# Optimization experiments

Measured on AMD Instinct MI355X. Metric: run time of the kernel, lower is better.

## Reference

```python
import jax, jax.numpy as jnp
import numpy as np

B, K = 524288, 64
CUTOFF = jnp.arange(K + 1, dtype=jnp.float32)  # len K+1
S0 = jnp.exp(jnp.float32(-4.0))                # s0 = exp(s0_init)
S = jnp.float32(2.0)                           # logit scale
M = jnp.float32(0.1)                           # margin
SIZE_LOSS = 'average'


def _get_labels(y, e):
    # bin b such that cutoff[b] <= y < cutoff[b+1]
    b = jnp.searchsorted(CUTOFF, y, side='right') - 1          # [B]
    valid = (b >= 0) & (b < K)                                 # [B]
    ar = jnp.arange(K)
    onehot = ar[None, :] == b[:, None]                         # event: single bin
    tail = ar[None, :] >= b[:, None]                           # censored: bin and all later bins
    count = jnp.where(e[:, None] != 0, onehot, tail) & valid[:, None]
    return count.astype(jnp.float32)                           # [B, K] in {0,1}


def setup_inputs() -> dict:
    key = jax.random.key(0)
    k1, k2, k3 = jax.random.split(key, 3)
    inp = jax.random.normal(k1, (B, K), dtype=jnp.float32)
    y = jax.random.uniform(k2, (B,), dtype=jnp.float32, minval=0.0, maxval=float(K))
    e = jax.random.randint(k3, (B,), 0, 2).astype(jnp.int32)
    return {'input': inp, 'y': y, 'e': e}


def reference(input, y, e):
    count = _get_labels(y, e)                                  # [B, K]
    # margin added where count[j] == min(count) (the 'negative' bins)
    min_c = jnp.min(count, axis=1, keepdims=True)
    logits = (input + M * (count == min_c).astype(input.dtype)) * S
    rev = 1.0 - count
    pe = jnp.exp(-logits)                                      # exp(-x)
    pen = jnp.exp(logits)                                      # exp(x)
    correct = jnp.sum(pe * count, axis=1)
    false_ev = jnp.sum(pen * rev, axis=1)
    false_cs = jnp.sum(pe * rev, axis=1)
    loss_ev = jnp.log(correct + S0) + jnp.log(false_ev + S0)
    loss_cs = jnp.log(1.0 + correct * false_cs + false_cs / S0)
    is_event_case = jnp.sum(count, axis=1) == 1.0
    per_sample = jnp.where(is_event_case, loss_ev, loss_cs)
    batch_loss = jnp.mean(per_sample) if SIZE_LOSS == 'average' else jnp.sum(per_sample)
    return batch_loss, count.astype(jnp.int32)
```

## Files before the change

kernel.cpp:

```cpp
#include <hip/hip_runtime.h>

#define BROWS 524288
#define KBINS 64
#define GRID1 2048
#define ITERS (BROWS / (GRID1 * 32))

typedef float v4f __attribute__((ext_vector_type(4)));

__global__ __launch_bounds__(256) void surv_main(
    const float* __restrict__ inp, const float* __restrict__ yv,
    const int* __restrict__ ev, float* __restrict__ out,
    float* __restrict__ partials)
{
  const int tid  = threadIdx.x;
  const int lane = tid & 63;
  const int wave = tid >> 6;
  const int sub  = lane >> 4;
  const int l16  = lane & 15;

  const float A   = 2.8853900817779268f;
  const float M2  = 0.28853900817779268f;
  const float S0  = 0.018315638888734179f;
  const float IS0 = 54.598150033144236f;
  const float LN2 = 0.6931471805599453f;

  float acc = 0.f;

  for (int it = 0; it < ITERS; ++it) {
    const int base = (it * GRID1 + blockIdx.x) * 32 + wave * 8;
    const int row0 = base + sub;
    const int row1 = base + 4 + sub;

    const int rp0 = row0 ? row0 - 1 : 0;
    const int rp1 = row1 - 1;
    const float y0 = yv[row0], y1 = yv[row1];
    const int   e0 = ev[row0], e1 = ev[row1];
    const float yp0 = yv[rp0], yp1 = yv[rp1];
    const int   ep0 = ev[rp0], ep1 = ev[rp1];
    const float4 x0 = *reinterpret_cast<const float4*>(
        inp + (size_t)row0 * KBINS + l16 * 4);
    const float4 x1 = *reinterpret_cast<const float4*>(
        inp + (size_t)row1 * KBINS + l16 * 4);

    #pragma unroll
    for (int h = 0; h < 2; ++h) {
      const int   row = h ? row1 : row0;
      const float y   = h ? y1 : y0;
      const int   e   = h ? e1 : e0;
      const float yp  = h ? yp1 : yp0;
      const int   ep  = h ? ep1 : ep0;
      const float4 x  = h ? x1 : x0;

      const int   b = (int)y;
      const bool valid = (y >= 0.f) && (y < 64.f);
      const int b_eff = valid ? b : 127;
      const int hi    = (e != 0) ? b_eff : 63;
      const bool all1 = (e == 0) && (b_eff == 0);
      const float m_in = all1 ? M2 : 0.f;

      const int   bp = (int)yp;
      const bool  vp = (yp >= 0.f) && (yp < 64.f);
      const float c63p = (ep != 0) ? ((vp && bp == 63) ? 1.f : 0.f)
                                   : (vp ? 1.f : 0.f);

      const float xa[4] = {x.x, x.y, x.z, x.w};
      float correct = 0.f, fev = 0.f, fcs = 0.f;
      float c[4];
      #pragma unroll
      for (int j = 0; j < 4; ++j) {
        const int bin = l16 * 4 + j;
        const bool cb = (bin >= b_eff) && (bin <= hi);
        const float mm = cb ? m_in : M2;
        const float t  = fmaf(xa[j], A, mm);
        const float pen = __builtin_amdgcn_exp2f(t);
        const float pe  = __builtin_amdgcn_exp2f(-t);
        correct += cb ? pe  : 0.f;
        fcs     += cb ? 0.f : pe;
        fev     += cb ? 0.f : pen;
        c[j] = cb ? 1.f : 0.f;
      }

      {
        const int binm1 = l16 * 4 - 1;
        const bool cm1 = (binm1 >= b_eff) && (binm1 <= hi);
        v4f cv;
        cv[0] = (l16 == 0) ? c63p : (cm1 ? 1.f : 0.f);
        cv[1] = c[0];
        cv[2] = c[1];
        cv[3] = c[2];
        *reinterpret_cast<v4f*>(out + (size_t)row * KBINS + l16 * 4) = cv;
        if (row == BROWS - 1 && l16 == 15)
          out[(size_t)BROWS * KBINS] = c[3];
      }

      #pragma unroll
      for (int m = 1; m < 16; m <<= 1) {
        correct += __shfl_xor(correct, m, 64);
        fev     += __shfl_xor(fev, m, 64);
        fcs     += __shfl_xor(fcs, m, 64);
      }

      const bool is_event = valid && (e != 0 || b == KBINS - 1);
      const float lev = (__builtin_amdgcn_logf(correct + S0) +
                         __builtin_amdgcn_logf(fev + S0)) * LN2;
      const float lcs = __builtin_amdgcn_logf(
                            fmaf(fcs, IS0, fmaf(correct, fcs, 1.f))) * LN2;
      if (l16 == 0) acc += is_event ? lev : lcs;
    }
  }

  acc += __shfl_xor(acc, 16, 64);
  acc += __shfl_xor(acc, 32, 64);
  __shared__ float sm[4];
  if (lane == 0) sm[wave] = acc;
  __syncthreads();
  if (tid == 0) partials[blockIdx.x] = (sm[0] + sm[1]) + (sm[2] + sm[3]);
}

__global__ __launch_bounds__(256) void surv_reduce(
    const float* __restrict__ partials, float* __restrict__ out)
{
  __shared__ float sm[256];
  float s = 0.f;
  for (int i = threadIdx.x; i < GRID1; i += 256) s += partials[i];
  sm[threadIdx.x] = s;
  __syncthreads();
  for (int o = 128; o > 0; o >>= 1) {
    if (threadIdx.x < o) sm[threadIdx.x] += sm[threadIdx.x + o];
    __syncthreads();
  }
  if (threadIdx.x == 0) out[0] = sm[0] * (1.0f / (float)BROWS);
}

extern "C" void kernel_launch(void* const* d_in, const int* in_sizes, int n_in,
                              void* d_out, int out_size, void* d_ws, size_t ws_size,
                              hipStream_t stream) {
  const float* inp = (const float*)d_in[0];
  const float* y   = (const float*)d_in[1];
  const int*   e   = (const int*)d_in[2];
  float* out      = (float*)d_out;
  float* partials = (float*)d_ws;

  surv_main<<<GRID1, 256, 0, stream>>>(inp, y, e, out, partials);
  surv_reduce<<<1, 256, 0, stream>>>(partials, out);
}
```

Before: 52.21 us.

## Software-pipeline input loads, share y/e via shuffles, fuse reduction via atomic

Each block now handles 64 rows per iteration. The next row's input vector is prefetched while the current one is computed, and y/e are loaded once per 16 rows and broadcast with wave shuffles instead of being reloaded per row. The separate reduce kernel is removed: each block adds a fixed-point partial into a 64-bit counter that also carries a block count, and the last block writes the mean. This costs a memset launch and a fixed-point quantisation of the partial sums, which assumes bounded per-block values.

```diff
diff --git a/kernel.cpp b/kernel.cpp
--- a/kernel.cpp
+++ b/kernel.cpp
@@ -3,14 +3,15 @@
 #define BROWS 524288
 #define KBINS 64
 #define GRID1 2048
-#define ITERS (BROWS / (GRID1 * 32))
+#define RPB   64
+#define ITERS (BROWS / (GRID1 * RPB))
 
 typedef float v4f __attribute__((ext_vector_type(4)));
 
 __global__ __launch_bounds__(256) void surv_main(
     const float* __restrict__ inp, const float* __restrict__ yv,
     const int* __restrict__ ev, float* __restrict__ out,
-    float* __restrict__ partials)
+    unsigned long long* __restrict__ acc64)
 {
   const int tid  = threadIdx.x;
   const int lane = tid & 63;
@@ -26,44 +27,54 @@
 
   float acc = 0.f;
 
+  {
+  }
+  int pf_row = blockIdx.x * RPB + wave * 16 + sub;
+  v4f xA = *reinterpret_cast<const v4f*>(inp + (size_t)pf_row * KBINS + l16 * 4);
+
   for (int it = 0; it < ITERS; ++it) {
-    const int base = (it * GRID1 + blockIdx.x) * 32 + wave * 8;
-    const int row0 = base + sub;
-    const int row1 = base + 4 + sub;
+    const int base = (it * GRID1 + blockIdx.x) * RPB + wave * 16;
 
-    const int rp0 = row0 ? row0 - 1 : 0;
-    const int rp1 = row1 - 1;
-    const float y0 = yv[row0], y1 = yv[row1];
-    const int   e0 = ev[row0], e1 = ev[row1];
-    const float yp0 = yv[rp0], yp1 = yv[rp1];
-    const int   ep0 = ev[rp0], ep1 = ev[rp1];
-    const float4 x0 = *reinterpret_cast<const float4*>(
-        inp + (size_t)row0 * KBINS + l16 * 4);
-    const float4 x1 = *reinterpret_cast<const float4*>(
-        inp + (size_t)row1 * KBINS + l16 * 4);
+    const float y_all = yv[base + l16];
+    const int   e_all = ev[base + l16];
+    const int   bm1 = (base > 0) ? base - 1 : 0;
+    const float ym1 = yv[bm1];
+    const int   em1 = ev[bm1];
+
+    const bool  v_all   = (y_all >= 0.f) && (y_all < 64.f);
+    const float c63_all = (e_all != 0) ? ((v_all && y_all >= 63.f) ? 1.f : 0.f)
+                                       : (v_all ? 1.f : 0.f);
+    const bool  vm1   = (ym1 >= 0.f) && (ym1 < 64.f);
+    const float c63m1 = (em1 != 0) ? ((vm1 && ym1 >= 63.f) ? 1.f : 0.f)
+                                   : (vm1 ? 1.f : 0.f);
 
     #pragma unroll
-    for (int h = 0; h < 2; ++h) {
-      const int   row = h ? row1 : row0;
-      const float y   = h ? y1 : y0;
-      const int   e   = h ? e1 : e0;
-      const float yp  = h ? yp1 : yp0;
-      const int   ep  = h ? ep1 : ep0;
-      const float4 x  = h ? x1 : x0;
+    for (int h = 0; h < 4; ++h) {
+      int nrow;
+      if (h < 3) {
+        nrow = base + (h + 1) * 4 + sub;
+      } else {
+        nrow = ((it + 1) * GRID1 + blockIdx.x) * RPB + wave * 16 + sub;
+        if (nrow >= BROWS) nrow = BROWS - 1;
+      }
+      const v4f xB = *reinterpret_cast<const v4f*>(
+          inp + (size_t)nrow * KBINS + l16 * 4);
 
-      const int   b = (int)y;
+      const int g   = h * 4 + sub;
+      const int row = base + g;
+      const float y = __shfl(y_all, g, 64);
+      const int   e = __shfl(e_all, g, 64);
+      const float c63w = __shfl(c63_all, g - 1, 64);
+      const float c63p = (g == 0) ? c63m1 : c63w;
+
+      const int  b = (int)y;
       const bool valid = (y >= 0.f) && (y < 64.f);
-      const int b_eff = valid ? b : 127;
-      const int hi    = (e != 0) ? b_eff : 63;
-      const bool all1 = (e == 0) && (b_eff == 0);
+      const int  b_eff = valid ? b : 127;
+      const int  hi    = (e != 0) ? b_eff : 63;
+      const bool all1  = (e == 0) && (b_eff == 0);
       const float m_in = all1 ? M2 : 0.f;
 
-      const int   bp = (int)yp;
-      const bool  vp = (yp >= 0.f) && (yp < 64.f);
-      const float c63p = (ep != 0) ? ((vp && bp == 63) ? 1.f : 0.f)
-                                   : (vp ? 1.f : 0.f);
-
-      const float xa[4] = {x.x, x.y, x.z, x.w};
+      const float xa[4] = {xA.x, xA.y, xA.z, xA.w};
       float correct = 0.f, fev = 0.f, fcs = 0.f;
       float c[4];
       #pragma unroll
@@ -81,14 +92,17 @@
       }
 
       {
-        const int binm1 = l16 * 4 - 1;
+        const int  binm1 = l16 * 4 - 1;
         const bool cm1 = (binm1 >= b_eff) && (binm1 <= hi);
         v4f cv;
         cv[0] = (l16 == 0) ? c63p : (cm1 ? 1.f : 0.f);
-        cv[1] = c[0];
-        cv[2] = c[1];
-        cv[3] = c[2];
-        *reinterpret_cast<v4f*>(out + (size_t)row * KBINS + l16 * 4) = cv;
+        cv[1] = c[0]; cv[2] = c[1]; cv[3] = c[2];
+        float* dst = out + (size_t)row * KBINS + l16 * 4;
+        if (row == 0 && l16 == 0) {
+          out[1] = cv[1]; out[2] = cv[2]; out[3] = cv[3];
+        } else {
+          *reinterpret_cast<v4f*>(dst) = cv;
+        }
         if (row == BROWS - 1 && l16 == 15)
           out[(size_t)BROWS * KBINS] = c[3];
       }
@@ -106,6 +120,8 @@
       const float lcs = __builtin_amdgcn_logf(
                             fmaf(fcs, IS0, fmaf(correct, fcs, 1.f))) * LN2;
       if (l16 == 0) acc += is_event ? lev : lcs;
+
+      xA = xB;
     }
   }
 
@@ -114,22 +130,19 @@
   __shared__ float sm[4];
   if (lane == 0) sm[wave] = acc;
   __syncthreads();
-  if (tid == 0) partials[blockIdx.x] = (sm[0] + sm[1]) + (sm[2] + sm[3]);
-}
-
-__global__ __launch_bounds__(256) void surv_reduce(
-    const float* __restrict__ partials, float* __restrict__ out)
-{
-  __shared__ float sm[256];
-  float s = 0.f;
-  for (int i = threadIdx.x; i < GRID1; i += 256) s += partials[i];
-  sm[threadIdx.x] = s;
-  __syncthreads();
-  for (int o = 128; o > 0; o >>= 1) {
-    if (threadIdx.x < o) sm[threadIdx.x] += sm[threadIdx.x + o];
-    __syncthreads();
+  if (tid == 0) {
+    const float partial = (sm[0] + sm[1]) + (sm[2] + sm[3]);
+    const unsigned long long fx =
+        (unsigned long long)((partial + 2100.0f) * 262144.0f + 0.5f);
+    const unsigned long long mine = (1ULL << 52) + fx;
+    const unsigned long long old  = atomicAdd(acc64, mine);
+    const unsigned long long tot  = old + mine;
+    if ((tot >> 52) == (unsigned long long)GRID1) {
+      const double s = (double)(tot & ((1ULL << 52) - 1)) * (1.0 / 262144.0)
+                     - 2100.0 * (double)GRID1;
+      out[0] = (float)(s / (double)BROWS);
+    }
   }
-  if (threadIdx.x == 0) out[0] = sm[0] * (1.0f / (float)BROWS);
 }
 
 extern "C" void kernel_launch(void* const* d_in, const int* in_sizes, int n_in,
@@ -138,9 +151,9 @@
   const float* inp = (const float*)d_in[0];
   const float* y   = (const float*)d_in[1];
   const int*   e   = (const int*)d_in[2];
-  float* out      = (float*)d_out;
-  float* partials = (float*)d_ws;
+  float* out = (float*)d_out;
+  unsigned long long* acc64 = (unsigned long long*)d_ws;
 
-  surv_main<<<GRID1, 256, 0, stream>>>(inp, y, e, out, partials);
-  surv_reduce<<<1, 256, 0, stream>>>(partials, out);
+  hipMemsetAsync(acc64, 0, sizeof(unsigned long long), stream);
+  surv_main<<<GRID1, 256, 0, stream>>>(inp, y, e, out, acc64);
 }
```

Measured after the change: 58.51 us. +12.1%, slower.
